# Performance work log

Hardware: AMD Instinct MI355X
Metric: run time of the kernel (lower is better)

The kernel has to match this reference:

```python
import jax, jax.numpy as jnp
import numpy as np

B = 16384
L = 128   # l_output_dim
H = 64    # hidden_dim
CTX = 16  # task_ctx_dim
DIMS = [2048, 167, 768, 512, 768, 300]  # RDK, MACCS, MolT5, MolCLR, UniMolV2_84M, GraphMVP
N = len(DIMS)


def setup_inputs() -> dict:
    key = jax.random.key(0)
    ks = jax.random.split(key, 64)
    names = ["x_rdk", "x_maccs", "x_molt5", "x_molclr", "x_unimol", "x_gmvp"]
    inp = {}
    for i, (n, d) in enumerate(zip(names, DIMS)):
        inp[n] = jax.random.normal(ks[i], (B, d), dtype=jnp.float32)
    inp["task_context"] = jax.random.normal(ks[10], (B, CTX), dtype=jnp.float32)
    # per-branch projection Linear(d -> L), stored as [d, L] for x @ W + b
    for i, d in enumerate(DIMS):
        s = 1.0 / np.sqrt(d)
        inp[f"Wp{i}"] = jax.random.uniform(ks[12 + i], (d, L), jnp.float32, -s, s)
        inp[f"bp{i}"] = jax.random.uniform(ks[20 + i], (L,), jnp.float32, -s, s)
    # attention MLP: Linear(L->H), ReLU, Linear(H->1)
    s1 = 1.0 / np.sqrt(L)
    inp["W1"] = jax.random.uniform(ks[30], (L, H), jnp.float32, -s1, s1)
    inp["b1"] = jax.random.uniform(ks[31], (H,), jnp.float32, -s1, s1)
    s2 = 1.0 / np.sqrt(H)
    inp["W2"] = jax.random.uniform(ks[32], (H, 1), jnp.float32, -s2, s2)
    inp["b2"] = jax.random.uniform(ks[33], (1,), jnp.float32, -s2, s2)
    inp["comp_beta"] = jnp.asarray(1.0, dtype=jnp.float32)
    # scalar task gate: Linear(CTX -> N)
    sg = 1.0 / np.sqrt(CTX)
    inp["Wg"] = jax.random.uniform(ks[34], (CTX, N), jnp.float32, -sg, sg)
    inp["bg"] = jax.random.uniform(ks[35], (N,), jnp.float32, -sg, sg)
    return inp


def reference(x_rdk, x_maccs, x_molt5, x_molclr, x_unimol, x_gmvp, task_context,
              Wp0, bp0, Wp1, bp1, Wp2, bp2, Wp3, bp3, Wp4, bp4, Wp5, bp5,
              W1, b1, W2, b2, comp_beta, Wg, bg):
    xs = [x_rdk, x_maccs, x_molt5, x_molclr, x_unimol, x_gmvp]
    Wps = [Wp0, Wp1, Wp2, Wp3, Wp4, Wp5]
    bps = [bp0, bp1, bp2, bp3, bp4, bp5]
    # per-branch projection to L dims
    projs = [x @ W + b for x, W, b in zip(xs, Wps, bps)]
    embeds = jnp.stack(projs, axis=1)  # [B, N, L]
    # validity mask per (sample, branch)
    norms = jnp.linalg.norm(embeds, axis=-1)  # [B, N]
    valid = (~jnp.isnan(embeds).any(axis=-1)) & (norms > 1e-8)  # [B, N]
    # attention MLP score
    h = jax.nn.relu(embeds @ W1 + b1)          # [B, N, H]
    scores = h @ W2 + b2                        # [B, N, 1]
    # cosine complementarity: comp[b, n] = mean_m (1 - cos(proj_n, proj_m))
    normed = embeds / jnp.maximum(norms[..., None], 1e-12)
    cos_sim = jnp.einsum('bnd,bmd->bnm', normed, normed)  # [B, N, N]
    comp_vec = jnp.mean(1.0 - cos_sim, axis=-1, keepdims=True)  # [B, N, 1]
    scores = scores + comp_beta * comp_vec
    # task-aware scalar gate bias
    task_bias = (task_context @ Wg + bg)[:, :, None]  # [B, N, 1]
    scores = scores + task_bias
    # masked softmax over branches
    scores = jnp.where(valid[:, :, None], scores, jnp.float32(-1e9))
    attn_weights = jax.nn.softmax(scores, axis=1)  # [B, N, 1]
    fused = jnp.sum(attn_weights * embeds, axis=1)  # [B, L]
    # dropout is identity (eval mode), sparse_lambda=0 -> sparse_reg omitted
    return fused
```

## Files before the change

### kernel.cpp

```cpp
#include <hip/hip_runtime.h>

typedef _Float16 half8 __attribute__((ext_vector_type(8)));
typedef float    floatx4 __attribute__((ext_vector_type(4)));

#define EMB_BYTES 25165824u

extern "C" __global__ __launch_bounds__(256) void k_prep(
    const float* __restrict__ Wp0, const float* __restrict__ Wp1,
    const float* __restrict__ Wp2, const float* __restrict__ Wp3,
    const float* __restrict__ Wp4, const float* __restrict__ Wp5,
    _Float16* __restrict__ Wt)
{
  const int DPAD_[6] = {2048,192,768,512,768,320};
  int j = blockIdx.x*256 + threadIdx.x;
  int i = 0, st = 0, cum = 0;
  #pragma unroll
  for (int q = 0; q < 6; q++){
    int sz = DPAD_[q] << 4;
    if (j >= cum){ i = q; st = cum; }
    cum += sz;
  }
  int local = j - st;
  int kc = local >> 7;
  int c  = local & 127;
  const float* Wp; int d, dpad, woff;
  switch(i){
    case 0:  Wp=Wp0; d=2048; dpad=2048; woff=0;      break;
    case 1:  Wp=Wp1; d=167;  dpad=192;  woff=262144; break;
    case 2:  Wp=Wp2; d=768;  dpad=768;  woff=286720; break;
    case 3:  Wp=Wp3; d=512;  dpad=512;  woff=385024; break;
    case 4:  Wp=Wp4; d=768;  dpad=768;  woff=450560; break;
    default: Wp=Wp5; d=300;  dpad=320;  woff=548864; break;
  }
  half8 h;
  #pragma unroll
  for (int u = 0; u < 8; u++){
    int k = (kc<<3) + u;
    float v = (k < d) ? Wp[(size_t)k*128 + c] : 0.0f;
    h[u] = (_Float16)v;
  }
  *(half8*)(Wt + woff + (size_t)c*dpad + (kc<<3)) = h;
}

__device__ __forceinline__ void load_a8(const float* __restrict__ xrow,
                                        int kb, int d, bool vec, float* a)
{
  if (vec && (kb + 8 <= d)){
    const float4* p = reinterpret_cast<const float4*>(xrow + kb);
    float4 v0 = p[0], v1 = p[1];
    a[0]=v0.x; a[1]=v0.y; a[2]=v0.z; a[3]=v0.w;
    a[4]=v1.x; a[5]=v1.y; a[6]=v1.z; a[7]=v1.w;
  } else {
    #pragma unroll
    for (int u = 0; u < 8; u++){
      int k = kb + u;
      a[u] = (k < d) ? xrow[k] : 0.0f;
    }
  }
}

__device__ __forceinline__ void cvt_store_a8(const float* a, _Float16* dst)
{
  half8 h;
  #pragma unroll
  for (int u = 0; u < 8; u++) h[u] = (_Float16)a[u];
  *(half8*)(dst) = h;
}

extern "C" __global__ __launch_bounds__(256, 5) void k_proj(
    const float* __restrict__ x0, const float* __restrict__ x1,
    const float* __restrict__ x2, const float* __restrict__ x3,
    const float* __restrict__ x4, const float* __restrict__ x5,
    const float* __restrict__ bp0, const float* __restrict__ bp1,
    const float* __restrict__ bp2, const float* __restrict__ bp3,
    const float* __restrict__ bp4, const float* __restrict__ bp5,
    const _Float16* __restrict__ Wt, _Float16* __restrict__ Eo)
{
  __shared__ _Float16 sA[2][64][40];

  int bl = blockIdx.x;
  int i, mtile;
  if      (bl <  256){ i=0; mtile=bl;      }
  else if (bl <  512){ i=2; mtile=bl-256;  }
  else if (bl <  768){ i=4; mtile=bl-512;  }
  else if (bl < 1024){ i=3; mtile=bl-768;  }
  else if (bl < 1280){ i=5; mtile=bl-1024; }
  else               { i=1; mtile=bl-1280; }

  const float* x; const float* bp; int d, dpad, woff;
  switch(i){
    case 0:  x=x0; bp=bp0; d=2048; dpad=2048; woff=0;      break;
    case 1:  x=x1; bp=bp1; d=167;  dpad=192;  woff=262144; break;
    case 2:  x=x2; bp=bp2; d=768;  dpad=768;  woff=286720; break;
    case 3:  x=x3; bp=bp3; d=512;  dpad=512;  woff=385024; break;
    case 4:  x=x4; bp=bp4; d=768;  dpad=768;  woff=450560; break;
    default: x=x5; bp=bp5; d=300;  dpad=320;  woff=548864; break;
  }
  int NT = dpad >> 5;
  bool vec = ((d & 3) == 0);
  const _Float16* wt = Wt + woff;
  int row0 = mtile << 6;

  int t = threadIdx.x;
  int lane = t & 63, wid = t >> 6;
  int wr = wid >> 1, wc = wid & 1;
  int l15 = lane & 15, l4 = lane >> 4;
  int srow = t >> 2;
  int koff = (t & 3) << 3;
  const float* xrow = x + (size_t)(row0 + srow)*d;

  const _Float16* bbase[4];
  #pragma unroll
  for (int nt = 0; nt < 4; nt++)
    bbase[nt] = wt + (size_t)((wc<<6) + (nt<<4) + l15)*dpad + (l4<<3);

  floatx4 acc[2][4];
  #pragma unroll
  for (int a_ = 0; a_ < 2; a_++)
    #pragma unroll
    for (int b_ = 0; b_ < 4; b_++)
      #pragma unroll
      for (int q = 0; q < 4; q++) acc[a_][b_][q] = 0.0f;

  {
    float a0[8];
    load_a8(xrow, koff, d, vec, a0);
    cvt_store_a8(a0, &sA[0][srow][koff]);
  }
  __syncthreads();

  for (int kt = 0; kt < NT; kt++){
    int cur = kt & 1;
    bool more = (kt + 1) < NT;
    float anx[8];
    if (more) load_a8(xrow, ((kt+1)<<5) + koff, d, vec, anx);
    half8 bf[4];
    #pragma unroll
    for (int nt = 0; nt < 4; nt++)
      bf[nt] = *(const half8*)(bbase[nt] + (kt<<5));
    #pragma unroll
    for (int mtl = 0; mtl < 2; mtl++){
      half8 af = *(const half8*)&sA[cur][(wr<<5)+(mtl<<4)+l15][l4<<3];
      #pragma unroll
      for (int nt = 0; nt < 4; nt++)
        acc[mtl][nt] = __builtin_amdgcn_mfma_f32_16x16x32_f16(af, bf[nt], acc[mtl][nt], 0, 0, 0);
    }
    if (more) cvt_store_a8(anx, &sA[cur^1][srow][koff]);
    __syncthreads();
  }

  #pragma unroll
  for (int nt = 0; nt < 4; nt++){
    int col = (wc<<6) + (nt<<4) + l15;
    float bv = bp[col];
    #pragma unroll
    for (int mtl = 0; mtl < 2; mtl++){
      int rbase = row0 + (wr<<5) + (mtl<<4) + (l4<<2);
      #pragma unroll
      for (int j = 0; j < 4; j++){
        float v = acc[mtl][nt][j] + bv;
        Eo[(size_t)(rbase + j)*768 + i*128 + col] = (_Float16)v;
      }
    }
  }
}

extern "C" __global__ __launch_bounds__(256) void k_attn(
    const _Float16* __restrict__ E,
    const float* __restrict__ W1, const float* __restrict__ b1,
    const float* __restrict__ W2, const float* __restrict__ b2,
    const float* __restrict__ beta_,
    const float* __restrict__ Wg, const float* __restrict__ bg,
    const float* __restrict__ ctx, float* __restrict__ out)
{
  __shared__ _Float16 eb[192][136];
  __shared__ _Float16 w1t[64][136];
  __shared__ float s_s1[192];
  __shared__ float s_gate[192];

  int t = threadIdx.x;
  int row0 = blockIdx.x << 5;
  int lane = t & 63, wid = t >> 6;
  int l15 = lane & 15, l4 = lane >> 4;

  {
    const _Float16* src = E + (size_t)row0*768;
    #pragma unroll
    for (int jj = 0; jj < 12; jj++){
      int off8 = t + (jj<<8);
      half8 v = *(const half8*)(src + ((size_t)off8<<3));
      int mrow = off8 >> 4; int kq = off8 & 15;
      *(half8*)&eb[mrow][kq<<3] = v;
    }
    #pragma unroll
    for (int jj = 0; jj < 8; jj++){
      int idx4 = t + (jj<<8);
      float4 v = *(const float4*)(W1 + ((size_t)idx4<<2));
      int k = idx4 >> 4; int h4 = (idx4 & 15) << 2;
      w1t[h4  ][k] = (_Float16)v.x;
      w1t[h4+1][k] = (_Float16)v.y;
      w1t[h4+2][k] = (_Float16)v.z;
      w1t[h4+3][k] = (_Float16)v.w;
    }
    if (t < 192){
      int r = t / 6; int n = t - r*6;
      const float* cr = ctx + (size_t)(row0 + r)*16;
      float g = bg[n];
      #pragma unroll
      for (int k = 0; k < 16; k++) g += cr[k] * Wg[k*6 + n];
      s_gate[t] = g;
    }
  }
  __syncthreads();

  {
    floatx4 acc[3][4];
    #pragma unroll
    for (int a_ = 0; a_ < 3; a_++)
      #pragma unroll
      for (int b_ = 0; b_ < 4; b_++)
        #pragma unroll
        for (int q = 0; q < 4; q++) acc[a_][b_][q] = 0.0f;

    #pragma unroll
    for (int ks = 0; ks < 4; ks++){
      half8 bf[4];
      #pragma unroll
      for (int nt = 0; nt < 4; nt++)
        bf[nt] = *(const half8*)&w1t[(nt<<4)+l15][(ks<<5)+(l4<<3)];
      #pragma unroll
      for (int m3 = 0; m3 < 3; m3++){
        half8 af = *(const half8*)&eb[wid*48 + (m3<<4) + l15][(ks<<5)+(l4<<3)];
        #pragma unroll
        for (int nt = 0; nt < 4; nt++)
          acc[m3][nt] = __builtin_amdgcn_mfma_f32_16x16x32_f16(af, bf[nt], acc[m3][nt], 0, 0, 0);
      }
    }
    float vb1[4], vw2[4];
    #pragma unroll
    for (int nt = 0; nt < 4; nt++){
      int col = (nt<<4) + l15;
      vb1[nt] = b1[col]; vw2[nt] = W2[col];
    }
    float b2v = b2[0];
    #pragma unroll
    for (int m3 = 0; m3 < 3; m3++){
      #pragma unroll
      for (int j = 0; j < 4; j++){
        float p = 0.0f;
        #pragma unroll
        for (int nt = 0; nt < 4; nt++){
          float v = acc[m3][nt][j] + vb1[nt];
          v = fmaxf(v, 0.0f);
          p += v * vw2[nt];
        }
        p += __shfl_xor(p, 1); p += __shfl_xor(p, 2);
        p += __shfl_xor(p, 4); p += __shfl_xor(p, 8);
        if (l15 == 0) s_s1[wid*48 + (m3<<4) + (l4<<2) + j] = p + b2v;
      }
    }
  }
  __syncthreads();

  {
    float BETA = beta_[0];
    for (int rr = 0; rr < 8; rr++){
      int lrow = (wid<<3) + rr;
      float e0[6], e1[6];
      #pragma unroll
      for (int n = 0; n < 6; n++){
        e0[n] = (float)eb[lrow*6+n][lane];
        e1[n] = (float)eb[lrow*6+n][64+lane];
      }
      float red[21];
      int c = 0;
      #pragma unroll
      for (int n = 0; n < 6; n++) red[c++] = e0[n]*e0[n] + e1[n]*e1[n];
      #pragma unroll
      for (int n = 0; n < 6; n++){
        #pragma unroll
        for (int m = n+1; m < 6; m++) red[c++] = e0[n]*e0[m] + e1[n]*e1[m];
      }
      #pragma unroll
      for (int q = 0; q < 21; q++){
        float v = red[q];
        v += __shfl_xor(v, 1);  v += __shfl_xor(v, 2);  v += __shfl_xor(v, 4);
        v += __shfl_xor(v, 8);  v += __shfl_xor(v, 16); v += __shfl_xor(v, 32);
        red[q] = v;
      }
      float den[6]; bool val[6];
      #pragma unroll
      for (int n = 0; n < 6; n++){
        val[n] = red[n] > 1e-16f;
        den[n] = fmaxf(sqrtf(red[n]), 1e-12f);
      }
      float csum[6];
      #pragma unroll
      for (int n = 0; n < 6; n++) csum[n] = red[n] / (den[n]*den[n]);
      {
        int cc = 6;
        #pragma unroll
        for (int n = 0; n < 6; n++){
          #pragma unroll
          for (int m = n+1; m < 6; m++){
            float cv = red[cc++] / (den[n]*den[m]);
            csum[n] += cv; csum[m] += cv;
          }
        }
      }
      float sc[6];
      #pragma unroll
      for (int n = 0; n < 6; n++){
        float comp = 1.0f - csum[n]*(1.0f/6.0f);
        float s = s_s1[lrow*6+n] + BETA*comp + s_gate[lrow*6+n];
        sc[n] = val[n] ? s : -1e9f;
      }
      float mx = sc[0];
      #pragma unroll
      for (int n = 1; n < 6; n++) mx = fmaxf(mx, sc[n]);
      float wsum = 0.0f; float w[6];
      #pragma unroll
      for (int n = 0; n < 6; n++){ w[n] = __expf(sc[n]-mx); wsum += w[n]; }
      float inv = 1.0f / wsum;
      float f0 = 0.0f, f1 = 0.0f;
      #pragma unroll
      for (int n = 0; n < 6; n++){
        float wn = w[n]*inv;
        f0 += wn*e0[n]; f1 += wn*e1[n];
      }
      size_t ob = (size_t)(row0 + lrow)*128;
      out[ob + lane]      = f0;
      out[ob + 64 + lane] = f1;
    }
  }
}

extern "C" void kernel_launch(void* const* d_in, const int* in_sizes, int n_in,
                              void* d_out, int out_size, void* d_ws, size_t ws_size,
                              hipStream_t stream)
{
  const float* x0 = (const float*)d_in[0];
  const float* x1 = (const float*)d_in[1];
  const float* x2 = (const float*)d_in[2];
  const float* x3 = (const float*)d_in[3];
  const float* x4 = (const float*)d_in[4];
  const float* x5 = (const float*)d_in[5];
  const float* ctx = (const float*)d_in[6];
  const float* Wp0 = (const float*)d_in[7];  const float* bp0 = (const float*)d_in[8];
  const float* Wp1 = (const float*)d_in[9];  const float* bp1 = (const float*)d_in[10];
  const float* Wp2 = (const float*)d_in[11]; const float* bp2 = (const float*)d_in[12];
  const float* Wp3 = (const float*)d_in[13]; const float* bp3 = (const float*)d_in[14];
  const float* Wp4 = (const float*)d_in[15]; const float* bp4 = (const float*)d_in[16];
  const float* Wp5 = (const float*)d_in[17]; const float* bp5 = (const float*)d_in[18];
  const float* W1 = (const float*)d_in[19];
  const float* b1 = (const float*)d_in[20];
  const float* W2 = (const float*)d_in[21];
  const float* b2 = (const float*)d_in[22];
  const float* beta = (const float*)d_in[23];
  const float* Wg = (const float*)d_in[24];
  const float* bg = (const float*)d_in[25];

  _Float16* ws_e = (_Float16*)d_ws;
  _Float16* Wt   = (_Float16*)((char*)d_ws + EMB_BYTES);
  float* outp = (float*)d_out;

  k_prep<<<288, 256, 0, stream>>>(Wp0, Wp1, Wp2, Wp3, Wp4, Wp5, Wt);
  k_proj<<<1536, 256, 0, stream>>>(x0, x1, x2, x3, x4, x5,
                                   bp0, bp1, bp2, bp3, bp4, bp5, Wt, ws_e);
  k_attn<<<512, 256, 0, stream>>>(ws_e, W1, b1, W2, b2, beta, Wg, bg, ctx, outp);
}
```

Baseline: 445.7 us.

## Stage 256-wide K chunks of x in LDS with coalesced row loads

Replaces the per-32-K double-buffered A staging with 256-wide K chunks: each wave loads whole row segments with contiguous float4 lanes, converts them to fp16 into a larger padded LDS tile, then runs eight MFMA K-steps from LDS. B fragments are software-prefetched one K-step ahead in registers. The aim is fully coalesced reads of x and fewer barriers per K. The cost is more LDS per block, occupancy lowered from 5 to 4, and no overlap between global loads and MFMA within a chunk.

```diff
diff --git a/kernel.cpp b/kernel.cpp
--- a/kernel.cpp
+++ b/kernel.cpp
@@ -1,6 +1,7 @@
 #include <hip/hip_runtime.h>
 
 typedef _Float16 half8 __attribute__((ext_vector_type(8)));
+typedef _Float16 half4 __attribute__((ext_vector_type(4)));
 typedef float    floatx4 __attribute__((ext_vector_type(4)));
 
 #define EMB_BYTES 25165824u
@@ -42,32 +43,7 @@
   *(half8*)(Wt + woff + (size_t)c*dpad + (kc<<3)) = h;
 }
 
-__device__ __forceinline__ void load_a8(const float* __restrict__ xrow,
-                                        int kb, int d, bool vec, float* a)
-{
-  if (vec && (kb + 8 <= d)){
-    const float4* p = reinterpret_cast<const float4*>(xrow + kb);
-    float4 v0 = p[0], v1 = p[1];
-    a[0]=v0.x; a[1]=v0.y; a[2]=v0.z; a[3]=v0.w;
-    a[4]=v1.x; a[5]=v1.y; a[6]=v1.z; a[7]=v1.w;
-  } else {
-    #pragma unroll
-    for (int u = 0; u < 8; u++){
-      int k = kb + u;
-      a[u] = (k < d) ? xrow[k] : 0.0f;
-    }
-  }
-}
-
-__device__ __forceinline__ void cvt_store_a8(const float* a, _Float16* dst)
-{
-  half8 h;
-  #pragma unroll
-  for (int u = 0; u < 8; u++) h[u] = (_Float16)a[u];
-  *(half8*)(dst) = h;
-}
-
-extern "C" __global__ __launch_bounds__(256, 5) void k_proj(
+extern "C" __global__ __launch_bounds__(256, 4) void k_proj(
     const float* __restrict__ x0, const float* __restrict__ x1,
     const float* __restrict__ x2, const float* __restrict__ x3,
     const float* __restrict__ x4, const float* __restrict__ x5,
@@ -76,7 +52,7 @@
     const float* __restrict__ bp4, const float* __restrict__ bp5,
     const _Float16* __restrict__ Wt, _Float16* __restrict__ Eo)
 {
-  __shared__ _Float16 sA[2][64][40];
+  __shared__ _Float16 sA[64][260];
 
   int bl = blockIdx.x;
   int i, mtile;
@@ -87,27 +63,22 @@
   else if (bl < 1280){ i=5; mtile=bl-1024; }
   else               { i=1; mtile=bl-1280; }
 
-  const float* x; const float* bp; int d, dpad, woff;
+  const float* x; const float* bp; int d, dpad, woff, nch;
   switch(i){
-    case 0:  x=x0; bp=bp0; d=2048; dpad=2048; woff=0;      break;
-    case 1:  x=x1; bp=bp1; d=167;  dpad=192;  woff=262144; break;
-    case 2:  x=x2; bp=bp2; d=768;  dpad=768;  woff=286720; break;
-    case 3:  x=x3; bp=bp3; d=512;  dpad=512;  woff=385024; break;
-    case 4:  x=x4; bp=bp4; d=768;  dpad=768;  woff=450560; break;
-    default: x=x5; bp=bp5; d=300;  dpad=320;  woff=548864; break;
-  }
-  int NT = dpad >> 5;
-  bool vec = ((d & 3) == 0);
+    case 0:  x=x0; bp=bp0; d=2048; dpad=2048; woff=0;      nch=8; break;
+    case 1:  x=x1; bp=bp1; d=167;  dpad=192;  woff=262144; nch=1; break;
+    case 2:  x=x2; bp=bp2; d=768;  dpad=768;  woff=286720; nch=3; break;
+    case 3:  x=x3; bp=bp3; d=512;  dpad=512;  woff=385024; nch=2; break;
+    case 4:  x=x4; bp=bp4; d=768;  dpad=768;  woff=450560; nch=3; break;
+    default: x=x5; bp=bp5; d=300;  dpad=320;  woff=548864; nch=2; break;
+  }
   const _Float16* wt = Wt + woff;
   int row0 = mtile << 6;
 
   int t = threadIdx.x;
-  int lane = t & 63, wid = t >> 6;
-  int wr = wid >> 1, wc = wid & 1;
+  int lane = t & 63, w = t >> 6;
+  int wr = w >> 1, wc = w & 1;
   int l15 = lane & 15, l4 = lane >> 4;
-  int srow = t >> 2;
-  int koff = (t & 3) << 3;
-  const float* xrow = x + (size_t)(row0 + srow)*d;
 
   const _Float16* bbase[4];
   #pragma unroll
@@ -122,30 +93,61 @@
       #pragma unroll
       for (int q = 0; q < 4; q++) acc[a_][b_][q] = 0.0f;
 
-  {
-    float a0[8];
-    load_a8(xrow, koff, d, vec, a0);
-    cvt_store_a8(a0, &sA[0][srow][koff]);
-  }
-  __syncthreads();
-
-  for (int kt = 0; kt < NT; kt++){
-    int cur = kt & 1;
-    bool more = (kt + 1) < NT;
-    float anx[8];
-    if (more) load_a8(xrow, ((kt+1)<<5) + koff, d, vec, anx);
-    half8 bf[4];
+  for (int kc = 0; kc < nch; kc++){
+    int kbase = kc << 8;
+
+    half8 bfn[4];
     #pragma unroll
     for (int nt = 0; nt < 4; nt++)
-      bf[nt] = *(const half8*)(bbase[nt] + (kt<<5));
-    #pragma unroll
-    for (int mtl = 0; mtl < 2; mtl++){
-      half8 af = *(const half8*)&sA[cur][(wr<<5)+(mtl<<4)+l15][l4<<3];
+      bfn[nt] = *(const half8*)(bbase[nt] + kbase);
+
+    #pragma unroll
+    for (int b = 0; b < 4; b++){
+      float4 v[4];
+      #pragma unroll
+      for (int j = 0; j < 4; j++){
+        int r = (w<<4) + (b<<2) + j;
+        int k = kbase + (lane<<2);
+        const float* p = x + (size_t)(row0 + r)*d + k;
+        if (k + 4 <= d) v[j] = *(const float4*)p;
+        else {
+          v[j].x = (k   < d) ? p[0] : 0.0f;
+          v[j].y = (k+1 < d) ? p[1] : 0.0f;
+          v[j].z = (k+2 < d) ? p[2] : 0.0f;
+          v[j].w = (k+3 < d) ? p[3] : 0.0f;
+        }
+      }
+      #pragma unroll
+      for (int j = 0; j < 4; j++){
+        int r = (w<<4) + (b<<2) + j;
+        half4 h;
+        h[0] = (_Float16)v[j].x; h[1] = (_Float16)v[j].y;
+        h[2] = (_Float16)v[j].z; h[3] = (_Float16)v[j].w;
+        *(half4*)&sA[r][lane<<2] = h;
+      }
+    }
+    __syncthreads();
+
+    int rem = dpad - kbase; if (rem > 256) rem = 256;
+    int NS = rem >> 5;
+    for (int ks = 0; ks < NS; ks++){
+      half8 bfc[4];
+      #pragma unroll
+      for (int nt = 0; nt < 4; nt++) bfc[nt] = bfn[nt];
+      if (ks + 1 < NS){
+        #pragma unroll
+        for (int nt = 0; nt < 4; nt++)
+          bfn[nt] = *(const half8*)(bbase[nt] + kbase + ((ks+1)<<5));
+      }
+      half8 af0 = *(const half8*)&sA[(wr<<5) + l15     ][(ks<<5)+(l4<<3)];
+      half8 af1 = *(const half8*)&sA[(wr<<5) + 16 + l15][(ks<<5)+(l4<<3)];
       #pragma unroll
       for (int nt = 0; nt < 4; nt++)
-        acc[mtl][nt] = __builtin_amdgcn_mfma_f32_16x16x32_f16(af, bf[nt], acc[mtl][nt], 0, 0, 0);
-    }
-    if (more) cvt_store_a8(anx, &sA[cur^1][srow][koff]);
+        acc[0][nt] = __builtin_amdgcn_mfma_f32_16x16x32_f16(af0, bfc[nt], acc[0][nt], 0, 0, 0);
+      #pragma unroll
+      for (int nt = 0; nt < 4; nt++)
+        acc[1][nt] = __builtin_amdgcn_mfma_f32_16x16x32_f16(af1, bfc[nt], acc[1][nt], 0, 0, 0);
+    }
     __syncthreads();
   }
 
```

After: 492.5 us. 10.5% more time.
